# Performance work log

Measured on AMD Instinct MI355X. Metric: run time of the kernel, lower is better.

## Reference

```python
import jax, jax.numpy as jnp
import numpy as np
from jax import lax

BIG = 1e6  # sentinel 1D distance when no zero seen yet (squared stays finite in fp32)


def edt_2d(binary):
    """Exact Euclidean distance transform of a (B, H, W) binary image.

    Matches scipy.ndimage.distance_transform_edt: for each nonzero pixel,
    distance to the nearest zero pixel. Separable formulation:
      pass 1: g[b,i,c]   = min_r |i - r| s.t. binary[b,r,c] == 0   (two scans)
      pass 2: d2[b,i,j]  = min_c g[b,i,c]^2 + (j - c)^2            (broadcast-min)
    """
    B, H, W = binary.shape
    xs = jnp.moveaxis(binary, 1, 0)  # (H, B, W) -> scan over rows

    def sweep(carry, x):
        d = jnp.where(x == 0, 0.0, carry + 1.0)
        return d, d

    init = jnp.full((B, W), BIG, dtype=binary.dtype)
    _, down = lax.scan(sweep, init, xs)
    _, up = lax.scan(sweep, init, xs, reverse=True)
    g = jnp.moveaxis(jnp.minimum(down, up), 0, 1)  # (B, H, W) vertical 1D EDT

    j = jnp.arange(W, dtype=binary.dtype)
    diff2 = (j[:, None] - j[None, :]) ** 2  # (W_out, W_src)
    # (B, H, 1, W) + (W, W) -> min over source column axis
    d2 = jnp.min(g[:, :, None, :] ** 2 + diff2[None, None, :, :], axis=-1)
    return jnp.sqrt(d2)


def combo_loss(pred, target,
               dice_weight=0.5, bce_weight=0.5, boundary_weight=0.1, focal_weight=0.2,
               smooth=1.0, alpha=1.0, gamma=2.0, inner_boundary_weight=1.0):
    p = jax.nn.sigmoid(pred)

    # Dice
    intersection = jnp.sum(p * target)
    union = jnp.sum(p) + jnp.sum(target)
    dice = 1.0 - (2.0 * intersection + smooth) / (union + smooth)

    # BCEWithLogits (stable)
    bce = jnp.mean(jnp.maximum(pred, 0.0) - pred * target
                   + jnp.log1p(jnp.exp(-jnp.abs(pred))))

    # Boundary loss (torch thresholds raw pred > 0.5, detached -> stop_gradient)
    pred_bin = lax.stop_gradient((pred > 0.5).astype(pred.dtype))[:, 0]    # (B,H,W)
    targ_bin = lax.stop_gradient(target.astype(pred.dtype))[:, 0]          # (B,H,W)
    # per-sample mean then batch mean == global mean (equal-size images)
    boundary = inner_boundary_weight * jnp.mean(
        jnp.abs(edt_2d(pred_bin) - edt_2d(targ_bin)))

    # Focal
    bce_el = -(target * jnp.log(p) + (1.0 - target) * jnp.log(1.0 - p))
    pt = p * target + (1.0 - p) * (1.0 - target)
    focal = jnp.mean(alpha * (1.0 - pt) ** gamma * bce_el)

    return (dice_weight * dice + bce_weight * bce
            + boundary_weight * boundary + focal_weight * focal)


def setup_inputs() -> dict:
    key = jax.random.key(0)
    k1, k2 = jax.random.split(key)
    B, C, H, W = 4, 1, 256, 256
    pred = jax.random.normal(k1, (B, C, H, W), dtype=jnp.float32)
    target = jax.random.bernoulli(k2, 0.5, (B, C, H, W)).astype(jnp.float32)
    return {"pred": pred, "target": target}


def reference(pred, target):
    return combo_loss(pred, target)
```

## Files before the change

kernel.cpp:

```cpp
#include <hip/hip_runtime.h>
#include <math.h>

#define BB 4
#define HH 256
#define WW 256
#define NN (BB*HH*WW)
typedef unsigned long long u64;

#define MASK_OFF_BYTES 256
#define SENT 100000

__global__ __launch_bounds__(128)
void build_masks(const float* __restrict__ pred,
                 const float* __restrict__ targ,
                 float* __restrict__ ws) {
    int t = blockIdx.x * 128 + threadIdx.x;
    if (t < 9) ws[t] = 0.0f;

    int c   = t & 255;
    int w   = (t >> 8) & 3;
    int b   = (t >> 10) & 3;
    int img = t >> 12;

    const float* s = (img ? targ : pred) + b * (HH * WW) + (w * 64) * WW + c;
    u64 m = 0;
    #pragma unroll
    for (int r = 0; r < 64; ++r) {
        float x = s[r * WW];
        m |= ((u64)(x <= 0.5f)) << r;
    }
    u64* maskT = (u64*)((char*)ws + MASK_OFF_BYTES);
    maskT[(((img * BB + b) * WW + c) << 2) + w] = m;
}

__global__ __launch_bounds__(256)
void band_fused(const float* __restrict__ pred,
                const float* __restrict__ targ,
                float* __restrict__ ws,
                float* __restrict__ out) {
    __shared__ float2 G[4][WW];
    __shared__ float red[4][6];
    __shared__ int amLast;

    int blk  = blockIdx.x;
    int b    = blk >> 6;
    int band = blk & 63;
    int i0   = band << 2;
    int wq   = i0 >> 6;
    int o0   = i0 & 63;
    int c    = threadIdx.x;

    const u64* maskT = (const u64*)((const char*)ws + MASK_OFF_BYTES);

    float g2v[2][4];
    #pragma unroll
    for (int img = 0; img < 2; ++img) {
        const u64* mp = maskT + (((img * BB + b) * WW + c) << 2);
        u64 M0 = mp[0], M1 = mp[1], M2 = mp[2], M3 = mp[3];

        int t1 = __ffsll(M1), t2 = __ffsll(M2), t3 = __ffsll(M3);
        int f1 = t1 ? 64 + t1 - 1  : SENT;
        int f2 = t2 ? 128 + t2 - 1 : SENT;
        int f3 = t3 ? 192 + t3 - 1 : SENT;
        int r0 = __ffsll(__brevll(M0));
        int r1 = __ffsll(__brevll(M1));
        int r2 = __ffsll(__brevll(M2));
        int l0 = r0 ? 64 - r0  : -SENT;
        int l1 = r1 ? 128 - r1 : -SENT;
        int l2 = r2 ? 192 - r2 : -SENT;

        int s3 = f3;
        int s2 = min(f2, s3);
        int s1 = min(f1, s2);
        int NF = (wq == 0) ? s1 : (wq == 1) ? s2 : (wq == 2) ? s3 : SENT;
        int q0 = l0;
        int q1 = max(q0, l1);
        int q2 = max(q1, l2);
        int PB = (wq == 0) ? -SENT : (wq == 1) ? q0 : (wq == 2) ? q1 : q2;
        u64 Mq = (wq == 0) ? M0 : (wq == 1) ? M1 : (wq == 2) ? M2 : M3;

        #pragma unroll
        for (int kk = 0; kk < 4; ++kk) {
            int i = i0 + kk, o = o0 + kk;
            u64 sh  = Mq >> o;
            int tn  = __ffsll(sh);
            int n   = tn ? i + tn - 1 : NF;
            u64 shl = Mq << (63 - o);
            int tp  = __ffsll(__brevll(shl));
            int p   = tp ? i - (tp - 1) : PB;
            int g   = min(n - i, i - p);
            g2v[img][kk] = (float)g * (float)g;
        }
    }
    #pragma unroll
    for (int kk = 0; kk < 4; ++kk)
        G[kk][c] = make_float2(g2v[0][kk], g2v[1][kk]);
    __syncthreads();

    int j = threadIdx.x;
    float d2p[4], d2t[4];
    #pragma unroll
    for (int k = 0; k < 4; ++k) {
        float2 g = G[k][j];
        d2p[k] = g.x; d2t[k] = g.y;
    }
    for (int r = 1; r < WW; ++r) {
        float r2 = (float)(r * r);
        float dmax = fmaxf(fmaxf(fmaxf(d2p[0], d2p[1]), fmaxf(d2p[2], d2p[3])),
                           fmaxf(fmaxf(d2t[0], d2t[1]), fmaxf(d2t[2], d2t[3])));
        if (__all(r2 >= dmax)) break;
        int lo = j - r, hi = j + r;
        if (lo >= 0) {
            #pragma unroll
            for (int k = 0; k < 4; ++k) {
                float2 g = G[k][lo];
                d2p[k] = fminf(d2p[k], g.x + r2);
                d2t[k] = fminf(d2t[k], g.y + r2);
            }
        }
        if (hi < WW) {
            #pragma unroll
            for (int k = 0; k < 4; ++k) {
                float2 g = G[k][hi];
                d2p[k] = fminf(d2p[k], g.x + r2);
                d2t[k] = fminf(d2t[k], g.y + r2);
            }
        }
    }

    float sPT = 0.0f, sP = 0.0f, sT = 0.0f, sBCE = 0.0f, sFOC = 0.0f, sBND = 0.0f;
    #pragma unroll
    for (int k = 0; k < 4; ++k) {
        int idx = (b * HH + (i0 + k)) * WW + j;
        float x = pred[idx];
        float t = targ[idx];

        sBND += fabsf(sqrtf(d2p[k]) - sqrtf(d2t[k]));

        float p   = 1.0f / (1.0f + expf(-x));
        float ax  = fabsf(x);
        float l1p = log1pf(expf(-ax));
        float bce_el = fmaxf(x, 0.0f) - x * t + l1p;
        float lsx  = fminf(x, 0.0f) - l1p;
        float lsnx = -fmaxf(x, 0.0f) - l1p;
        float bce_f = -(t * lsx + (1.0f - t) * lsnx);
        float pt = p * t + (1.0f - p) * (1.0f - t);
        float om = 1.0f - pt;

        sPT  += p * t;
        sP   += p;
        sT   += t;
        sBCE += bce_el;
        sFOC += om * om * bce_f;
    }

    float vals[6] = { sPT, sP, sT, sBCE, sFOC, sBND };
    int lane = threadIdx.x & 63;
    int wave = threadIdx.x >> 6;
    #pragma unroll
    for (int k = 0; k < 6; ++k) {
        float v = vals[k];
        #pragma unroll
        for (int off = 32; off > 0; off >>= 1)
            v += __shfl_down(v, off, 64);
        if (lane == 0) red[wave][k] = v;
    }
    __syncthreads();
    if (threadIdx.x < 6) {
        float s = red[0][threadIdx.x] + red[1][threadIdx.x]
                + red[2][threadIdx.x] + red[3][threadIdx.x];
        atomicAdd(&ws[threadIdx.x], s);
        __threadfence();
    }
    __syncthreads();

    if (threadIdx.x == 0) {
        unsigned old = atomicAdd((unsigned*)(ws + 6), 1u);
        amLast = (old == 255u);
    }
    __syncthreads();
    if (amLast && threadIdx.x == 0) {
        float inter = atomicAdd(&ws[0], 0.0f);
        float sp    = atomicAdd(&ws[1], 0.0f);
        float st    = atomicAdd(&ws[2], 0.0f);
        float bce   = atomicAdd(&ws[3], 0.0f);
        float foc   = atomicAdd(&ws[4], 0.0f);
        float bnd   = atomicAdd(&ws[5], 0.0f);
        float invN = 1.0f / (float)NN;
        float dice = 1.0f - (2.0f * inter + 1.0f) / (sp + st + 1.0f);
        out[0] = 0.5f * dice + 0.5f * (bce * invN)
               + 0.1f * (bnd * invN) + 0.2f * (foc * invN);
    }
}

extern "C" void kernel_launch(void* const* d_in, const int* in_sizes, int n_in,
                              void* d_out, int out_size, void* d_ws, size_t ws_size,
                              hipStream_t stream) {
    const float* pred = (const float*)d_in[0];
    const float* targ = (const float*)d_in[1];
    float* ws = (float*)d_ws;

    build_masks<<<64, 128, 0, stream>>>(pred, targ, ws);
    band_fused<<<BB * 64, 256, 0, stream>>>(pred, targ, ws, (float*)d_out);
}
```

Baseline: 70.15 us.

## Fuse mask build and band kernel into one launch with grid-wide flag barriers

Merges the mask-building kernel into the band kernel, so the whole loss runs in a single launch. Each block builds a slice of the bit masks, publishes a per-block magic flag, then computes the elementwise loss terms while the other blocks finish. It then spin-waits on all flags before the distance-transform step, and block 0 waits on a second set of flags to write the final value. This removes one kernel launch and hides the mask-build latency, but it requires all 256 blocks to be resident at the same time. Because the magic flags are never cleared, repeated calls can pass the barriers early and read stale masks or partially reset accumulators.

Result: slower. 118.0 us (+68.1%).

```diff
diff --git a/kernel.cpp b/kernel.cpp
--- a/kernel.cpp
+++ b/kernel.cpp
@@ -6,56 +6,93 @@
 #define WW 256
 #define NN (BB*HH*WW)
 typedef unsigned long long u64;
-
-#define MASK_OFF_BYTES 256
+typedef unsigned int u32;
+
+#define FLAG1_OFF 128
+#define FLAG2_OFF 1152
+#define MASK_OFF  4096
+#define MAGIC1 0x13579BDFu
+#define MAGIC2 0x2468ACE1u
 #define SENT 100000
 
-__global__ __launch_bounds__(128)
-void build_masks(const float* __restrict__ pred,
+__global__ __launch_bounds__(256)
+void combo_fused(const float* __restrict__ pred,
                  const float* __restrict__ targ,
-                 float* __restrict__ ws) {
-    int t = blockIdx.x * 128 + threadIdx.x;
-    if (t < 9) ws[t] = 0.0f;
-
-    int c   = t & 255;
-    int w   = (t >> 8) & 3;
-    int b   = (t >> 10) & 3;
-    int img = t >> 12;
-
-    const float* s = (img ? targ : pred) + b * (HH * WW) + (w * 64) * WW + c;
-    u64 m = 0;
-    #pragma unroll
-    for (int r = 0; r < 64; ++r) {
-        float x = s[r * WW];
-        m |= ((u64)(x <= 0.5f)) << r;
-    }
-    u64* maskT = (u64*)((char*)ws + MASK_OFF_BYTES);
-    maskT[(((img * BB + b) * WW + c) << 2) + w] = m;
-}
-
-__global__ __launch_bounds__(256)
-void band_fused(const float* __restrict__ pred,
-                const float* __restrict__ targ,
-                float* __restrict__ ws,
-                float* __restrict__ out) {
+                 float* __restrict__ ws,
+                 float* __restrict__ out) {
     __shared__ float2 G[4][WW];
     __shared__ float red[4][6];
-    __shared__ int amLast;
-
-    int blk  = blockIdx.x;
-    int b    = blk >> 6;
-    int band = blk & 63;
-    int i0   = band << 2;
-    int wq   = i0 >> 6;
-    int o0   = i0 & 63;
-    int c    = threadIdx.x;
-
-    const u64* maskT = (const u64*)((const char*)ws + MASK_OFF_BYTES);
-
+
+    const int blk = blockIdx.x;
+    const int tid = threadIdx.x;
+    u32* flag1 = (u32*)((char*)ws + FLAG1_OFF);
+    u32* flag2 = (u32*)((char*)ws + FLAG2_OFF);
+    u64* maskT = (u64*)((char*)ws + MASK_OFF);
+
+    if (tid < 32) {
+        int t   = blk * 32 + tid;
+        int c   = t & 255;
+        int w   = (t >> 8) & 3;
+        int b   = (t >> 10) & 3;
+        int img = t >> 12;
+        const float* s = (img ? targ : pred) + b * (HH * WW) + (w * 64) * WW + c;
+        u64 m = 0;
+        #pragma unroll
+        for (int r = 0; r < 64; ++r) {
+            float x = s[r * WW];
+            m |= ((u64)(x <= 0.5f)) << r;
+        }
+        maskT[(((img * BB + b) * WW + c) << 2) + w] = m;
+    }
+    if (blk == 0 && tid < 6) ws[tid] = 0.0f;
+    __threadfence();
+    __syncthreads();
+    if (tid == 0)
+        __hip_atomic_store(&flag1[blk], MAGIC1, __ATOMIC_RELEASE, __HIP_MEMORY_SCOPE_AGENT);
+
+    const int b    = blk >> 6;
+    const int band = blk & 63;
+    const int i0   = band << 2;
+    const int j    = tid;
+
+    float sPT = 0.0f, sP = 0.0f, sT = 0.0f, sBCE = 0.0f, sFOC = 0.0f, sBND = 0.0f;
+    #pragma unroll
+    for (int k = 0; k < 4; ++k) {
+        int idx = (b * HH + (i0 + k)) * WW + j;
+        float x = pred[idx];
+        float t = targ[idx];
+
+        float p   = 1.0f / (1.0f + expf(-x));
+        float ax  = fabsf(x);
+        float l1p = log1pf(expf(-ax));
+        float bce_el = fmaxf(x, 0.0f) - x * t + l1p;
+        float lsx  = fminf(x, 0.0f) - l1p;
+        float lsnx = -fmaxf(x, 0.0f) - l1p;
+        float bce_f = -(t * lsx + (1.0f - t) * lsnx);
+        float pt = p * t + (1.0f - p) * (1.0f - t);
+        float om = 1.0f - pt;
+
+        sPT  += p * t;
+        sP   += p;
+        sT   += t;
+        sBCE += bce_el;
+        sFOC += om * om * bce_f;
+    }
+
+    {
+        bool ok;
+        do {
+            u32 v = __hip_atomic_load(&flag1[tid], __ATOMIC_ACQUIRE, __HIP_MEMORY_SCOPE_AGENT);
+            ok = (v == MAGIC1);
+        } while (!__syncthreads_and(ok));
+    }
+
+    const int wq = i0 >> 6;
+    const int o0 = i0 & 63;
     float g2v[2][4];
     #pragma unroll
     for (int img = 0; img < 2; ++img) {
-        const u64* mp = maskT + (((img * BB + b) * WW + c) << 2);
+        const u64* mp = maskT + (((img * BB + b) * WW + j) << 2);
         u64 M0 = mp[0], M1 = mp[1], M2 = mp[2], M3 = mp[3];
 
         int t1 = __ffsll(M1), t2 = __ffsll(M2), t3 = __ffsll(M3);
@@ -94,10 +131,9 @@
     }
     #pragma unroll
     for (int kk = 0; kk < 4; ++kk)
-        G[kk][c] = make_float2(g2v[0][kk], g2v[1][kk]);
-    __syncthreads();
-
-    int j = threadIdx.x;
+        G[kk][j] = make_float2(g2v[0][kk], g2v[1][kk]);
+    __syncthreads();
+
     float d2p[4], d2t[4];
     #pragma unroll
     for (int k = 0; k < 4; ++k) {
@@ -127,36 +163,13 @@
             }
         }
     }
-
-    float sPT = 0.0f, sP = 0.0f, sT = 0.0f, sBCE = 0.0f, sFOC = 0.0f, sBND = 0.0f;
-    #pragma unroll
-    for (int k = 0; k < 4; ++k) {
-        int idx = (b * HH + (i0 + k)) * WW + j;
-        float x = pred[idx];
-        float t = targ[idx];
-
+    #pragma unroll
+    for (int k = 0; k < 4; ++k)
         sBND += fabsf(sqrtf(d2p[k]) - sqrtf(d2t[k]));
 
-        float p   = 1.0f / (1.0f + expf(-x));
-        float ax  = fabsf(x);
-        float l1p = log1pf(expf(-ax));
-        float bce_el = fmaxf(x, 0.0f) - x * t + l1p;
-        float lsx  = fminf(x, 0.0f) - l1p;
-        float lsnx = -fmaxf(x, 0.0f) - l1p;
-        float bce_f = -(t * lsx + (1.0f - t) * lsnx);
-        float pt = p * t + (1.0f - p) * (1.0f - t);
-        float om = 1.0f - pt;
-
-        sPT  += p * t;
-        sP   += p;
-        sT   += t;
-        sBCE += bce_el;
-        sFOC += om * om * bce_f;
-    }
-
     float vals[6] = { sPT, sP, sT, sBCE, sFOC, sBND };
-    int lane = threadIdx.x & 63;
-    int wave = threadIdx.x >> 6;
+    int lane = tid & 63;
+    int wave = tid >> 6;
     #pragma unroll
     for (int k = 0; k < 6; ++k) {
         float v = vals[k];
@@ -166,30 +179,33 @@
         if (lane == 0) red[wave][k] = v;
     }
     __syncthreads();
-    if (threadIdx.x < 6) {
-        float s = red[0][threadIdx.x] + red[1][threadIdx.x]
-                + red[2][threadIdx.x] + red[3][threadIdx.x];
-        atomicAdd(&ws[threadIdx.x], s);
-        __threadfence();
-    }
-    __syncthreads();
-
-    if (threadIdx.x == 0) {
-        unsigned old = atomicAdd((unsigned*)(ws + 6), 1u);
-        amLast = (old == 255u);
-    }
-    __syncthreads();
-    if (amLast && threadIdx.x == 0) {
-        float inter = atomicAdd(&ws[0], 0.0f);
-        float sp    = atomicAdd(&ws[1], 0.0f);
-        float st    = atomicAdd(&ws[2], 0.0f);
-        float bce   = atomicAdd(&ws[3], 0.0f);
-        float foc   = atomicAdd(&ws[4], 0.0f);
-        float bnd   = atomicAdd(&ws[5], 0.0f);
-        float invN = 1.0f / (float)NN;
-        float dice = 1.0f - (2.0f * inter + 1.0f) / (sp + st + 1.0f);
-        out[0] = 0.5f * dice + 0.5f * (bce * invN)
-               + 0.1f * (bnd * invN) + 0.2f * (foc * invN);
+    if (tid < 6) {
+        float s = red[0][tid] + red[1][tid] + red[2][tid] + red[3][tid];
+        atomicAdd(&ws[tid], s);
+    }
+    __threadfence();
+    __syncthreads();
+    if (tid == 0)
+        __hip_atomic_store(&flag2[blk], MAGIC2, __ATOMIC_RELEASE, __HIP_MEMORY_SCOPE_AGENT);
+
+    if (blk == 0) {
+        bool ok;
+        do {
+            u32 v = __hip_atomic_load(&flag2[tid], __ATOMIC_ACQUIRE, __HIP_MEMORY_SCOPE_AGENT);
+            ok = (v == MAGIC2);
+        } while (!__syncthreads_and(ok));
+        if (tid == 0) {
+            float inter = atomicAdd(&ws[0], 0.0f);
+            float sp    = atomicAdd(&ws[1], 0.0f);
+            float st    = atomicAdd(&ws[2], 0.0f);
+            float bce   = atomicAdd(&ws[3], 0.0f);
+            float foc   = atomicAdd(&ws[4], 0.0f);
+            float bnd   = atomicAdd(&ws[5], 0.0f);
+            float invN = 1.0f / (float)NN;
+            float dice = 1.0f - (2.0f * inter + 1.0f) / (sp + st + 1.0f);
+            out[0] = 0.5f * dice + 0.5f * (bce * invN)
+                   + 0.1f * (bnd * invN) + 0.2f * (foc * invN);
+        }
     }
 }
 
@@ -198,8 +214,5 @@
                               hipStream_t stream) {
     const float* pred = (const float*)d_in[0];
     const float* targ = (const float*)d_in[1];
-    float* ws = (float*)d_ws;
-
-    build_masks<<<64, 128, 0, stream>>>(pred, targ, ws);
-    band_fused<<<BB * 64, 256, 0, stream>>>(pred, targ, ws, (float*)d_out);
+    combo_fused<<<BB * 64, 256, 0, stream>>>(pred, targ, (float*)d_ws, (float*)d_out);
 }
```
